# Kernel optimization log

Hardware: AMD Instinct MI355X
Metric: run time of the kernel (lower is better)

## Reference

```python
import jax, jax.numpy as jnp
import numpy as np

DIM, HEADS = 128, 8
DH = DIM // HEADS
SCALE = DH ** -0.5
N, E = 50000, 800000


def setup_inputs() -> dict:
    key = jax.random.key(0)
    ks = jax.random.split(key, 12)
    w = lambda k: jax.random.normal(k, (DIM, DIM), dtype=jnp.float32) * 0.02
    b = lambda k: jax.random.normal(k, (DIM,), dtype=jnp.float32) * 0.02
    return {
        "q_nodes": jax.random.normal(ks[0], (N, DIM), dtype=jnp.float32),
        "k_edges": jax.random.normal(ks[1], (E, DIM), dtype=jnp.float32),
        "v_edges": jax.random.normal(ks[2], (E, DIM), dtype=jnp.float32),
        "edge_index": jax.random.randint(ks[3], (2, E), 0, N, dtype=jnp.int64),
        "Wq": w(ks[4]), "bq": b(ks[5]),
        "Wk": w(ks[6]), "bk": b(ks[7]),
        "Wv": w(ks[8]), "bv": b(ks[9]),
        "Wo": w(ks[10]), "bo": b(ks[11]),
    }


def reference(q_nodes, k_edges, v_edges, edge_index, Wq, bq, Wk, bk, Wv, bv, Wo, bo):
    n, e = q_nodes.shape[0], k_edges.shape[0]
    dst = edge_index[0]  # src (edge_index[1]) is unused by the module
    q = (q_nodes @ Wq.T + bq).reshape(n, HEADS, DH)
    k = (k_edges @ Wk.T + bk).reshape(e, HEADS, DH)
    v = (v_edges @ Wv.T + bv).reshape(e, HEADS, DH)
    # per-edge score: dot(q[dst], k) per head -> [E, H]
    score = jnp.einsum('ehd,ehd->eh', q[dst], k) * SCALE
    # segment (per-dst-node) softmax over edges, numerically stable
    m = jax.ops.segment_max(score, dst, num_segments=n)          # [N, H]
    ex = jnp.exp(score - m[dst])                                  # [E, H]
    s = jax.ops.segment_sum(ex, dst, num_segments=n)             # [N, H]
    w = ex / (s[dst] + 1e-16)                                     # [E, H]
    weighted_v = (v * w[..., None]).reshape(e, DIM)               # [E, dim]
    aggr = jax.ops.segment_sum(weighted_v, dst, num_segments=n)  # [N, dim]
    return aggr @ Wo.T + bo
```

## Files before the change

### kernel.cpp

```cpp
#include <hip/hip_runtime.h>

#define TM 64
#define NTHREADS 256
#define PAD 132

typedef __attribute__((ext_vector_type(8))) short short8;
typedef __attribute__((ext_vector_type(4))) float f32x4;

__device__ __forceinline__ short f2bf(float f) {
  union { float f; unsigned u; } uf; uf.f = f;
  unsigned r = uf.u + 0x7FFFu + ((uf.u >> 16) & 1u);
  return (short)(r >> 16);
}
__device__ __forceinline__ float bf2f(short s) {
  union { unsigned u; float f; } uf; uf.u = ((unsigned)(unsigned short)s) << 16;
  return uf.f;
}
__device__ __forceinline__ short8 pack8(float4 a, float4 b) {
  short8 r;
  r[0] = f2bf(a.x); r[1] = f2bf(a.y); r[2] = f2bf(a.z); r[3] = f2bf(a.w);
  r[4] = f2bf(b.x); r[5] = f2bf(b.y); r[6] = f2bf(b.z); r[7] = f2bf(b.w);
  return r;
}


__global__ __launch_bounds__(512) void proj_mfma(
    const float* __restrict__ X, const short* __restrict__ Wb,
    const float* __restrict__ bias, float* __restrict__ Y, int M, float scale) {
  __shared__ short Xb[8192];
  int t = threadIdx.x;
  int w = t >> 6, l = t & 63, g = l >> 4, c = l & 15;
  short8 wf[4];
#pragma unroll
  for (int kc = 0; kc < 4; ++kc)
    wf[kc] = *(const short8*)(Wb + (w * 16 + c) * 128 + kc * 32 + g * 8);
  float4 b4 = *(const float4*)(bias + w * 16 + g * 4);

  for (int rb = blockIdx.x * 64; rb < M; rb += gridDim.x * 64) {
    {
      int r = t >> 3, q8 = t & 7;
      int row = rb + r; if (row >= M) row = M - 1;
      const float4* xs = (const float4*)(X + (size_t)row * 128 + q8 * 16);
      float4 x0 = xs[0], x1 = xs[1], x2 = xs[2], x3 = xs[3];
      int sw = (r & 7) << 4;
      *(short8*)((char*)Xb + r * 256 + ((q8 * 32) ^ sw)) = pack8(x0, x1);
      *(short8*)((char*)Xb + r * 256 + ((q8 * 32 + 16) ^ sw)) = pack8(x2, x3);
    }
    __syncthreads();
#pragma unroll
    for (int et = 0; et < 4; ++et) {
      int rl = et * 16 + c;
      f32x4 acc = {};
      int sw = (rl & 7) << 4;
#pragma unroll
      for (int kc = 0; kc < 4; ++kc) {
        short8 xb = *(const short8*)((char*)Xb + rl * 256 + ((kc * 64 + g * 16) ^ sw));
        acc = __builtin_amdgcn_mfma_f32_16x16x32_bf16(wf[kc], xb, acc, 0, 0, 0);
      }
      int row = rb + rl;
      if (row < M) {
        float4 o;
        o.x = (acc[0] + b4.x) * scale; o.y = (acc[1] + b4.y) * scale;
        o.z = (acc[2] + b4.z) * scale; o.w = (acc[3] + b4.w) * scale;
        *(float4*)(Y + (size_t)row * 128 + w * 16 + g * 4) = o;
      }
    }
    __syncthreads();
  }
}


__global__ __launch_bounds__(256) void hist_kernel(const int* __restrict__ dst,
                                                   int* __restrict__ cnt, int E) {
  int e = blockIdx.x * 256 + threadIdx.x;
  if (e < E) atomicAdd(&cnt[dst[e]], 1);
}

__global__ __launch_bounds__(1024) void scan_part(const int* __restrict__ cnt,
                                                  int* __restrict__ part, int N) {
  __shared__ int ws[16];
  int t = threadIdx.x, i = blockIdx.x * 1024 + t;
  int v = (i < N) ? cnt[i] : 0;
#pragma unroll
  for (int d = 1; d < 64; d <<= 1) v += __shfl_xor(v, d);
  if ((t & 63) == 0) ws[t >> 6] = v;
  __syncthreads();
  if (t < 16) {
    int x = ws[t];
#pragma unroll
    for (int d = 1; d < 16; d <<= 1) x += __shfl_xor(x, d);
    if (t == 0) part[blockIdx.x] = x;
  }
}

__global__ __launch_bounds__(64) void scan_offs(int* __restrict__ part, int P) {
  int t = threadIdx.x;
  int carry = 0;
  for (int base = 0; base < P; base += 64) {
    int i = base + t;
    int v = (i < P) ? part[i] : 0;
    int x = v;
#pragma unroll
    for (int d = 1; d < 64; d <<= 1) { int y = __shfl_up(x, d); if (t >= d) x += y; }
    if (i < P) part[i] = x - v + carry;
    carry += __shfl(x, 63);
  }
}

__global__ __launch_bounds__(1024) void scan_final(const int* __restrict__ cnt,
                                                   const int* __restrict__ part,
                                                   int* __restrict__ rp,
                                                   int* __restrict__ cur, int N) {
  __shared__ int ws[16];
  __shared__ int wofs[16];
  int t = threadIdx.x, i = blockIdx.x * 1024 + t;
  int lane = t & 63, wid = t >> 6;
  int v = (i < N) ? cnt[i] : 0;
  int x = v;
#pragma unroll
  for (int d = 1; d < 64; d <<= 1) { int y = __shfl_up(x, d); if (lane >= d) x += y; }
  if (lane == 63) ws[wid] = x;
  __syncthreads();
  if (t == 0) {
    int s = 0;
#pragma unroll
    for (int k2 = 0; k2 < 16; ++k2) { int tmp = ws[k2]; wofs[k2] = s; s += tmp; }
  }
  __syncthreads();
  int incl = x + wofs[wid] + part[blockIdx.x];
  int excl = incl - v;
  if (i < N) {
    rp[i] = excl; cur[i] = excl;
    if (i == N - 1) rp[N] = incl;
  }
}

__global__ __launch_bounds__(256) void perm_kernel(const int* __restrict__ dst,
                                                   int* __restrict__ cursor,
                                                   int* __restrict__ perm, int E) {
  int e = blockIdx.x * 256 + threadIdx.x;
  if (e < E) perm[e] = atomicAdd(&cursor[dst[e]], 1);
}

__global__ __launch_bounds__(256) void wprep4(
    const float* __restrict__ Wq, const float* __restrict__ Wk,
    const float* __restrict__ Wv, const float* __restrict__ Wo,
    short* __restrict__ wqb, short* __restrict__ wkb,
    short* __restrict__ wvb, short* __restrict__ wob) {
  int i = blockIdx.x * 256 + threadIdx.x;
  if (i < 16384) {
    wqb[i] = f2bf(Wq[i]); wkb[i] = f2bf(Wk[i]);
    wvb[i] = f2bf(Wv[i]); wob[i] = f2bf(Wo[i]);
  }
}


__global__ __launch_bounds__(512) void kproj_score(
    const float* __restrict__ K, const int* __restrict__ eidx,
    const int* __restrict__ perm, const short* __restrict__ wkb,
    const float* __restrict__ bk, const float* __restrict__ qp,
    float* __restrict__ exb, int E) {
  __shared__ short Kb[8192];
  int t = threadIdx.x;
  int w = t >> 6, l = t & 63, g = l >> 4, c = l & 15;
  short8 wK[4];
#pragma unroll
  for (int kc = 0; kc < 4; ++kc)
    wK[kc] = *(const short8*)(wkb + (w * 16 + c) * 128 + kc * 32 + g * 8);
  float4 bk4 = *(const float4*)(bk + w * 16 + g * 4);
  int r = t >> 3, q8 = t & 7;
  int b0 = r * 256 + ((q8 * 32) ^ ((r & 7) << 4));
  int stride = gridDim.x * 64;
  int eb = blockIdx.x * 64;

  float4 k0, k1, k2, k3;
  int d[4], p[4];
  {
    int row0 = eb + r; if (row0 >= E) row0 = E - 1;
    const float4* ks = (const float4*)(K + (size_t)row0 * 128 + q8 * 16);
    k0 = ks[0]; k1 = ks[1]; k2 = ks[2]; k3 = ks[3];
#pragma unroll
    for (int et = 0; et < 4; ++et) {
      int e = eb + et * 16 + c; if (e >= E) e = E - 1;
      d[et] = eidx[e]; p[et] = perm[e];
    }
  }

  for (; eb < E; eb += stride) {
    int ebn = eb + stride;
    bool hn = ebn < E;
    __syncthreads();
    *(short8*)((char*)Kb + b0) = pack8(k0, k1);
    *(short8*)((char*)Kb + (b0 ^ 16)) = pack8(k2, k3);
    float4 qv[4];
#pragma unroll
    for (int et = 0; et < 4; ++et)
      qv[et] = *(const float4*)(qp + (size_t)d[et] * 128 + w * 16 + g * 4);
    if (hn) {
      int rowk = ebn + r; if (rowk >= E) rowk = E - 1;
      const float4* ks = (const float4*)(K + (size_t)rowk * 128 + q8 * 16);
      k0 = ks[0]; k1 = ks[1]; k2 = ks[2]; k3 = ks[3];
    }
    int dn[4], pn[4];
    if (hn) {
#pragma unroll
      for (int et = 0; et < 4; ++et) {
        int e = ebn + et * 16 + c; if (e >= E) e = E - 1;
        dn[et] = eidx[e]; pn[et] = perm[e];
      }
    }
    __syncthreads();

#pragma unroll
    for (int et = 0; et < 4; ++et) {
      int eloc = et * 16 + c;
      int swr = (eloc & 7) << 4;
      f32x4 acc = {};
#pragma unroll
      for (int kc = 0; kc < 4; ++kc) {
        short8 xb = *(const short8*)((char*)Kb + eloc * 256 + ((kc * 64 + g * 16) ^ swr));
        acc = __builtin_amdgcn_mfma_f32_16x16x32_bf16(wK[kc], xb, acc, 0, 0, 0);
      }
      float s = (acc[0] + bk4.x) * qv[et].x + (acc[1] + bk4.y) * qv[et].y +
                (acc[2] + bk4.z) * qv[et].z + (acc[3] + bk4.w) * qv[et].w;
      s += __shfl_xor(s, 16);
      s += __shfl_xor(s, 32);
      if (g == 0) exb[(size_t)p[et] * 8 + w] = __expf(s);
    }
    if (hn) {
#pragma unroll
      for (int et = 0; et < 4; ++et) { d[et] = dn[et]; p[et] = pn[et]; }
    }
  }
}


__global__ __launch_bounds__(512) void vproj_weight(
    const float* __restrict__ V, const int* __restrict__ perm,
    const short* __restrict__ wvb, const float* __restrict__ exb,
    short* __restrict__ wv, int E) {
  __shared__ short Vb[8192];
  __shared__ short Ob[8192];
  int t = threadIdx.x;
  int w = t >> 6, l = t & 63, g = l >> 4, c = l & 15;
  short8 wV[4];
#pragma unroll
  for (int kc = 0; kc < 4; ++kc)
    wV[kc] = *(const short8*)(wvb + (w * 16 + c) * 128 + kc * 32 + g * 8);
  int r = t >> 3, q8 = t & 7;
  int b0 = r * 256 + ((q8 * 32) ^ ((r & 7) << 4));
  int stride = gridDim.x * 64;
  int eb = blockIdx.x * 64;

  float4 v0, v1, v2, v3;
  int p[4];
  {
    int row0 = eb + r; if (row0 >= E) row0 = E - 1;
    const float4* vs = (const float4*)(V + (size_t)row0 * 128 + q8 * 16);
    v0 = vs[0]; v1 = vs[1]; v2 = vs[2]; v3 = vs[3];
#pragma unroll
    for (int et = 0; et < 4; ++et) {
      int e = eb + et * 16 + c; if (e >= E) e = E - 1;
      p[et] = perm[e];
    }
  }

  for (; eb < E; eb += stride) {
    int ebn = eb + stride;
    bool hn = ebn < E;
    __syncthreads();
    *(short8*)((char*)Vb + b0) = pack8(v0, v1);
    *(short8*)((char*)Vb + (b0 ^ 16)) = pack8(v2, v3);
    float ev[4];
#pragma unroll
    for (int et = 0; et < 4; ++et)
      ev[et] = exb[(size_t)p[et] * 8 + w];
    int erow = eb + r; if (erow >= E) erow = E - 1;
    int prow = perm[erow];
    if (hn) {
      int rowv = ebn + r; if (rowv >= E) rowv = E - 1;
      const float4* vs = (const float4*)(V + (size_t)rowv * 128 + q8 * 16);
      v0 = vs[0]; v1 = vs[1]; v2 = vs[2]; v3 = vs[3];
    }
    int pn[4];
    if (hn) {
#pragma unroll
      for (int et = 0; et < 4; ++et) {
        int e = ebn + et * 16 + c; if (e >= E) e = E - 1;
        pn[et] = perm[e];
      }
    }
    __syncthreads();

#pragma unroll
    for (int et = 0; et < 4; ++et) {
      int eloc = et * 16 + c;
      int swr = (eloc & 7) << 4;
      f32x4 acc = {};
#pragma unroll
      for (int kc = 0; kc < 4; ++kc) {
        short8 xb = *(const short8*)((char*)Vb + eloc * 256 + ((kc * 64 + g * 16) ^ swr));
        acc = __builtin_amdgcn_mfma_f32_16x16x32_bf16(wV[kc], xb, acc, 0, 0, 0);
      }
      short4 sv;
      sv.x = f2bf(acc[0] * ev[et]); sv.y = f2bf(acc[1] * ev[et]);
      sv.z = f2bf(acc[2] * ev[et]); sv.w = f2bf(acc[3] * ev[et]);
      *(short4*)((char*)Ob + eloc * 256 + ((w * 32 + g * 8) ^ swr)) = sv;
    }
    __syncthreads();

    {
      int sw = (r & 7) << 4;
      short8 a = *(const short8*)((char*)Ob + r * 256 + ((q8 * 32) ^ sw));
      short8 b = *(const short8*)((char*)Ob + r * 256 + ((q8 * 32 + 16) ^ sw));
      *(short8*)(wv + (size_t)prow * 128 + q8 * 16) = a;
      *(short8*)(wv + (size_t)prow * 128 + q8 * 16 + 8) = b;
    }
    if (hn) {
#pragma unroll
      for (int et = 0; et < 4; ++et) p[et] = pn[et];
    }
  }
}


__global__ __launch_bounds__(256) void pull3(
    const short* __restrict__ wv, const float* __restrict__ exb,
    const int* __restrict__ rp, const float* __restrict__ bv,
    float* __restrict__ aggr, int N) {
  int w = threadIdx.x >> 6, l = threadIdx.x & 63;
  int n = blockIdx.x * 4 + w;
  if (n >= N) return;
  int beg = rp[n], end = rp[n + 1];
  int h = l >> 3;
  float a0 = 0.f, a1 = 0.f, s = 0.f;
  int j = beg;
  for (; j + 1 < end; j += 2) {
    unsigned u0 = *(const unsigned*)(wv + (size_t)j * 128 + l * 2);
    unsigned u1 = *(const unsigned*)(wv + (size_t)(j + 1) * 128 + l * 2);
    float s0 = exb[(size_t)j * 8 + h], s1 = exb[(size_t)(j + 1) * 8 + h];
    a0 += bf2f((short)(u0 & 0xFFFFu)) + bf2f((short)(u1 & 0xFFFFu));
    a1 += bf2f((short)(u0 >> 16)) + bf2f((short)(u1 >> 16));
    s += s0 + s1;
  }
  if (j < end) {
    unsigned u0 = *(const unsigned*)(wv + (size_t)j * 128 + l * 2);
    s += exb[(size_t)j * 8 + h];
    a0 += bf2f((short)(u0 & 0xFFFFu));
    a1 += bf2f((short)(u0 >> 16));
  }
  float2 o;
  if (end > beg) {
    float inv = 1.f / (s + 1e-16f);
    float2 bvv = *(const float2*)(bv + l * 2);
    o.x = a0 * inv + bvv.x; o.y = a1 * inv + bvv.y;
  } else {
    o.x = 0.f; o.y = 0.f;
  }
  *(float2*)(aggr + (size_t)n * 128 + l * 2) = o;
}


__device__ __forceinline__ void stage_x(float (*Xs)[PAD], const float* __restrict__ X,
                                        int rowbase, int M, int t) {
#pragma unroll
  for (int i = 0; i < 8; ++i) {
    int idx = t + NTHREADS * i;
    int r = idx >> 5, q = idx & 31;
    int row = rowbase + r;
    if (row >= M) row = M - 1;
    const float4 v = *(const float4*)(X + (size_t)row * 128 + q * 4);
    *(float4*)(&Xs[r][q * 4]) = v;
  }
}

__device__ __forceinline__ void gemm_tile(const float (*Xs)[PAD], float (*WT)[PAD],
                                          const float* __restrict__ W,
                                          float acc[8][4], int r0, int c0, int t) {
#pragma unroll 1
  for (int kk = 0; kk < 128; kk += 32) {
    {
      int j = t >> 1, half = t & 1;
      const float* src = W + j * 128 + kk + half * 16;
      float4 a = *(const float4*)(src);
      float4 b = *(const float4*)(src + 4);
      float4 c = *(const float4*)(src + 8);
      float4 d = *(const float4*)(src + 12);
      int cb = half * 16;
      WT[cb + 0][j] = a.x;  WT[cb + 1][j] = a.y;  WT[cb + 2][j] = a.z;  WT[cb + 3][j] = a.w;
      WT[cb + 4][j] = b.x;  WT[cb + 5][j] = b.y;  WT[cb + 6][j] = b.z;  WT[cb + 7][j] = b.w;
      WT[cb + 8][j] = c.x;  WT[cb + 9][j] = c.y;  WT[cb + 10][j] = c.z; WT[cb + 11][j] = c.w;
      WT[cb + 12][j] = d.x; WT[cb + 13][j] = d.y; WT[cb + 14][j] = d.z; WT[cb + 15][j] = d.w;
    }
    __syncthreads();
#pragma unroll
    for (int c2 = 0; c2 < 16; ++c2) {
      float4 wa = *(const float4*)(&WT[2 * c2][c0]);
      float4 wb = *(const float4*)(&WT[2 * c2 + 1][c0]);
#pragma unroll
      for (int i = 0; i < 8; ++i) {
        float2 xv = *(const float2*)(&Xs[r0 + i][kk + 2 * c2]);
        acc[i][0] = fmaf(xv.x, wa.x, acc[i][0]);
        acc[i][1] = fmaf(xv.x, wa.y, acc[i][1]);
        acc[i][2] = fmaf(xv.x, wa.z, acc[i][2]);
        acc[i][3] = fmaf(xv.x, wa.w, acc[i][3]);
        acc[i][0] = fmaf(xv.y, wb.x, acc[i][0]);
        acc[i][1] = fmaf(xv.y, wb.y, acc[i][1]);
        acc[i][2] = fmaf(xv.y, wb.z, acc[i][2]);
        acc[i][3] = fmaf(xv.y, wb.w, acc[i][3]);
      }
    }
    __syncthreads();
  }
}

__global__ __launch_bounds__(NTHREADS) void proj_kernel(
    const float* __restrict__ X, const float* __restrict__ W,
    const float* __restrict__ b, float* __restrict__ Y, int M) {
  __shared__ float Xs[TM][PAD];
  __shared__ float WT[32][PAD];
  int t = threadIdx.x;
  int B0 = blockIdx.x * TM;
  stage_x(Xs, X, B0, M, t);
  __syncthreads();
  int r0 = (t >> 5) * 8, m = t & 31, c0 = m * 4;
  float acc[8][4] = {};
  gemm_tile(Xs, WT, W, acc, r0, c0, t);
  float4 bv = ((const float4*)b)[m];
#pragma unroll
  for (int i = 0; i < 8; ++i) {
    int row = B0 + r0 + i;
    if (row < M) {
      float4 o;
      o.x = acc[i][0] + bv.x; o.y = acc[i][1] + bv.y;
      o.z = acc[i][2] + bv.z; o.w = acc[i][3] + bv.w;
      *(float4*)(Y + (size_t)row * 128 + c0) = o;
    }
  }
}

__global__ __launch_bounds__(NTHREADS) void edge_kernel(
    const float* __restrict__ Kin, const float* __restrict__ Vin,
    const int* __restrict__ eidx,
    const float* __restrict__ Wk, const float* __restrict__ bk,
    const float* __restrict__ Wv, const float* __restrict__ bv,
    const float* __restrict__ qp, float* __restrict__ s_sum,
    float* __restrict__ aggr, int E) {
  __shared__ float Xs[TM][PAD];
  __shared__ float WT[32][PAD];
  __shared__ int dsts[TM];
  int t = threadIdx.x;
  int e0 = blockIdx.x * TM;
  if (t < TM) {
    int idx = e0 + t;
    if (idx >= E) idx = E - 1;
    dsts[t] = eidx[idx];
  }
  stage_x(Xs, Kin, e0, E, t);
  __syncthreads();
  int r0 = (t >> 5) * 8, m = t & 31, c0 = m * 4;
  int h = m >> 2;
  float acc[8][4] = {};
  gemm_tile(Xs, WT, Wk, acc, r0, c0, t);
  float4 bkv = ((const float4*)bk)[m];
  float ex[8];
#pragma unroll
  for (int i = 0; i < 8; ++i) {
    int r = r0 + i;
    const float4 qv = *(const float4*)(qp + (size_t)dsts[r] * 128 + c0);
    float p = (acc[i][0] + bkv.x) * qv.x + (acc[i][1] + bkv.y) * qv.y +
              (acc[i][2] + bkv.z) * qv.z + (acc[i][3] + bkv.w) * qv.w;
    p += __shfl_xor(p, 1);
    p += __shfl_xor(p, 2);
    float e = __expf(p * 0.25f);
    ex[i] = e;
    if ((m & 3) == 0 && (e0 + r) < E)
      atomicAdd(&s_sum[(size_t)dsts[r] * 8 + h], e);
  }
  __syncthreads();
  stage_x(Xs, Vin, e0, E, t);
  __syncthreads();
#pragma unroll
  for (int i = 0; i < 8; ++i)
#pragma unroll
    for (int j = 0; j < 4; ++j) acc[i][j] = 0.f;
  gemm_tile(Xs, WT, Wv, acc, r0, c0, t);
  float4 bvv = ((const float4*)bv)[m];
#pragma unroll
  for (int i = 0; i < 8; ++i) {
    int r = r0 + i;
    if ((e0 + r) < E) {
      size_t base = (size_t)dsts[r] * 128 + c0;
      atomicAdd(&aggr[base + 0], (acc[i][0] + bvv.x) * ex[i]);
      atomicAdd(&aggr[base + 1], (acc[i][1] + bvv.y) * ex[i]);
      atomicAdd(&aggr[base + 2], (acc[i][2] + bvv.z) * ex[i]);
      atomicAdd(&aggr[base + 3], (acc[i][3] + bvv.w) * ex[i]);
    }
  }
}

__global__ __launch_bounds__(NTHREADS) void out_kernel(
    const float* __restrict__ aggr, const float* __restrict__ s_sum,
    const float* __restrict__ W, const float* __restrict__ b,
    float* __restrict__ Y, int M) {
  __shared__ float Xs[TM][PAD];
  __shared__ float WT[32][PAD];
  int t = threadIdx.x;
  int B0 = blockIdx.x * TM;
#pragma unroll
  for (int i = 0; i < 8; ++i) {
    int idx = t + NTHREADS * i;
    int r = idx >> 5, q = idx & 31;
    int row = B0 + r;
    if (row >= M) row = M - 1;
    float4 v = *(const float4*)(aggr + (size_t)row * 128 + q * 4);
    float inv = 1.0f / (s_sum[(size_t)row * 8 + (q >> 2)] + 1e-16f);
    v.x *= inv; v.y *= inv; v.z *= inv; v.w *= inv;
    *(float4*)(&Xs[r][q * 4]) = v;
  }
  __syncthreads();
  int r0 = (t >> 5) * 8, m = t & 31, c0 = m * 4;
  float acc[8][4] = {};
  gemm_tile(Xs, WT, W, acc, r0, c0, t);
  float4 bv = ((const float4*)b)[m];
#pragma unroll
  for (int i = 0; i < 8; ++i) {
    int row = B0 + r0 + i;
    if (row < M) {
      float4 o;
      o.x = acc[i][0] + bv.x; o.y = acc[i][1] + bv.y;
      o.z = acc[i][2] + bv.z; o.w = acc[i][3] + bv.w;
      *(float4*)(Y + (size_t)row * 128 + c0) = o;
    }
  }
}


extern "C" void kernel_launch(void* const* d_in, const int* in_sizes, int n_in,
                              void* d_out, int out_size, void* d_ws, size_t ws_size,
                              hipStream_t stream) {
  const float* q_nodes = (const float*)d_in[0];
  const float* k_edges = (const float*)d_in[1];
  const float* v_edges = (const float*)d_in[2];
  const int* eidx = (const int*)d_in[3];
  const float* Wq = (const float*)d_in[4];
  const float* bq = (const float*)d_in[5];
  const float* Wk = (const float*)d_in[6];
  const float* bk = (const float*)d_in[7];
  const float* Wv = (const float*)d_in[8];
  const float* bv = (const float*)d_in[9];
  const float* Wo = (const float*)d_in[10];
  const float* bo = (const float*)d_in[11];

  int N = in_sizes[0] / 128;
  int E = in_sizes[1] / 128;
  int P = (N + 1023) / 1024;

  size_t off = 0;
  auto alloc = [&](size_t b) { size_t o = off; off += (b + 255) & ~(size_t)255; return o; };
  size_t o_qp   = alloc((size_t)N * 128 * 4);
  size_t o_aggr = alloc((size_t)N * 128 * 4);
  size_t o_exb  = alloc((size_t)E * 8 * 4);
  size_t o_rp   = alloc(((size_t)N + 1) * 4);
  size_t o_cur  = alloc((size_t)N * 4);
  size_t o_cnt  = alloc((size_t)N * 4);
  size_t o_perm = alloc((size_t)E * 4);
  size_t o_part = alloc((size_t)(P + 1) * 4);
  size_t o_wqb  = alloc((size_t)16384 * 2);
  size_t o_wkb  = alloc((size_t)16384 * 2);
  size_t o_wvb  = alloc((size_t)16384 * 2);
  size_t o_wob  = alloc((size_t)16384 * 2);
  size_t o_wv   = alloc((size_t)E * 128 * 2);

  if (off <= ws_size) {
    char* base = (char*)d_ws;
    float* qp    = (float*)(base + o_qp);
    float* aggr  = (float*)(base + o_aggr);
    float* exb   = (float*)(base + o_exb);
    int*   rp    = (int*)(base + o_rp);
    int*   cur   = (int*)(base + o_cur);
    int*   cnt   = (int*)(base + o_cnt);
    int*   perm  = (int*)(base + o_perm);
    int*   part  = (int*)(base + o_part);
    short* wqb   = (short*)(base + o_wqb);
    short* wkb   = (short*)(base + o_wkb);
    short* wvb   = (short*)(base + o_wvb);
    short* wob   = (short*)(base + o_wob);
    short* wvbuf = (short*)(base + o_wv);

    hipMemsetAsync(cnt, 0, (size_t)N * 4, stream);
    wprep4<<<64, 256, 0, stream>>>(Wq, Wk, Wv, Wo, wqb, wkb, wvb, wob);
    proj_mfma<<<(N + 63) / 64, 512, 0, stream>>>(q_nodes, wqb, bq, qp, N, 0.25f);
    hist_kernel<<<(E + 255) / 256, 256, 0, stream>>>(eidx, cnt, E);
    scan_part<<<P, 1024, 0, stream>>>(cnt, part, N);
    scan_offs<<<1, 64, 0, stream>>>(part, P);
    scan_final<<<P, 1024, 0, stream>>>(cnt, part, rp, cur, N);
    perm_kernel<<<(E + 255) / 256, 256, 0, stream>>>(eidx, cur, perm, E);

    int eblk = (E + 63) / 64; if (eblk > 1024) eblk = 1024;
    kproj_score<<<eblk, 512, 0, stream>>>(k_edges, eidx, perm, wkb, bk, qp, exb, E);
    vproj_weight<<<eblk, 512, 0, stream>>>(v_edges, perm, wvb, exb, wvbuf, E);
    pull3<<<(N + 3) / 4, 256, 0, stream>>>(wvbuf, exb, rp, bv, aggr, N);
    proj_mfma<<<(N + 63) / 64, 512, 0, stream>>>(aggr, wob, bo, (float*)d_out, N, 1.0f);
  } else {
    float* q_proj = (float*)d_ws;
    float* s_sum  = q_proj + (size_t)N * 128;
    float* aggr   = s_sum + (size_t)N * 8;
    hipMemsetAsync(s_sum, 0, (size_t)N * 136 * sizeof(float), stream);
    int nblk = (N + TM - 1) / TM;
    int eblk = (E + TM - 1) / TM;
    proj_kernel<<<nblk, NTHREADS, 0, stream>>>(q_nodes, Wq, bq, q_proj, N);
    edge_kernel<<<eblk, NTHREADS, 0, stream>>>(k_edges, v_edges, eidx, Wk, bk, Wv, bv,
                                               q_proj, s_sum, aggr, E);
    out_kernel<<<nblk, NTHREADS, 0, stream>>>(aggr, s_sum, Wo, bo, (float*)d_out, N);
  }
}
```

Baseline: 448.9 us.

## Fuse V projection with segment aggregation via sorted-order atomics and fold normalization into output GEMM

The V projection kernel now walks edges in destination-sorted order, gathering V rows through an inverse permutation. Within each 64-edge tile it reduces runs of equal destination nodes in shared memory and flushes them with float atomics into raw aggregate and sum buffers. This removes the bf16 weighted-V intermediate (E×128) and the separate pull kernel. Softmax normalization and the V bias move into the output projection's load stage. The cost is scattered V row gathers and atomic contention at tile boundaries, and float atomics make the summation order nondeterministic.

New measurement: 513.7 us. 14.4% more time.

```diff
diff --git a/kernel.cpp b/kernel.cpp
--- a/kernel.cpp
+++ b/kernel.cpp
@@ -62,6 +62,66 @@
         float4 o;
         o.x = (acc[0] + b4.x) * scale; o.y = (acc[1] + b4.y) * scale;
         o.z = (acc[2] + b4.z) * scale; o.w = (acc[3] + b4.w) * scale;
+        *(float4*)(Y + (size_t)row * 128 + w * 16 + g * 4) = o;
+      }
+    }
+    __syncthreads();
+  }
+}
+
+
+__global__ __launch_bounds__(512) void proj_out_norm(
+    const float* __restrict__ araw, const float* __restrict__ sraw,
+    const float* __restrict__ bvv, const short* __restrict__ Wb,
+    const float* __restrict__ bias, float* __restrict__ Y, int M) {
+  __shared__ short Xb[8192];
+  int t = threadIdx.x;
+  int w = t >> 6, l = t & 63, g = l >> 4, c = l & 15;
+  short8 wf[4];
+#pragma unroll
+  for (int kc = 0; kc < 4; ++kc)
+    wf[kc] = *(const short8*)(Wb + (w * 16 + c) * 128 + kc * 32 + g * 8);
+  float4 b4 = *(const float4*)(bias + w * 16 + g * 4);
+
+  for (int rb = blockIdx.x * 64; rb < M; rb += gridDim.x * 64) {
+    {
+      int r = t >> 3, q8 = t & 7;
+      int row = rb + r; if (row >= M) row = M - 1;
+      float s = sraw[(size_t)row * 8 + q8];
+      const float4* as = (const float4*)(araw + (size_t)row * 128 + q8 * 16);
+      const float4* bs = (const float4*)(bvv + q8 * 16);
+      float4 x0, x1, x2, x3;
+      if (s > 0.f) {
+        float inv = 1.f / (s + 1e-16f);
+        float4 a0 = as[0], a1 = as[1], a2 = as[2], a3 = as[3];
+        float4 c0 = bs[0], c1 = bs[1], c2 = bs[2], c3 = bs[3];
+        x0.x = a0.x*inv + c0.x; x0.y = a0.y*inv + c0.y; x0.z = a0.z*inv + c0.z; x0.w = a0.w*inv + c0.w;
+        x1.x = a1.x*inv + c1.x; x1.y = a1.y*inv + c1.y; x1.z = a1.z*inv + c1.z; x1.w = a1.w*inv + c1.w;
+        x2.x = a2.x*inv + c2.x; x2.y = a2.y*inv + c2.y; x2.z = a2.z*inv + c2.z; x2.w = a2.w*inv + c2.w;
+        x3.x = a3.x*inv + c3.x; x3.y = a3.y*inv + c3.y; x3.z = a3.z*inv + c3.z; x3.w = a3.w*inv + c3.w;
+      } else {
+        x0 = {0,0,0,0}; x1 = {0,0,0,0}; x2 = {0,0,0,0}; x3 = {0,0,0,0};
+      }
+      int sw = (r & 7) << 4;
+      *(short8*)((char*)Xb + r * 256 + ((q8 * 32) ^ sw)) = pack8(x0, x1);
+      *(short8*)((char*)Xb + r * 256 + ((q8 * 32 + 16) ^ sw)) = pack8(x2, x3);
+    }
+    __syncthreads();
+#pragma unroll
+    for (int et = 0; et < 4; ++et) {
+      int rl = et * 16 + c;
+      f32x4 acc = {};
+      int sw = (rl & 7) << 4;
+#pragma unroll
+      for (int kc = 0; kc < 4; ++kc) {
+        short8 xb = *(const short8*)((char*)Xb + rl * 256 + ((kc * 64 + g * 16) ^ sw));
+        acc = __builtin_amdgcn_mfma_f32_16x16x32_bf16(wf[kc], xb, acc, 0, 0, 0);
+      }
+      int row = rb + rl;
+      if (row < M) {
+        float4 o;
+        o.x = acc[0] + b4.x; o.y = acc[1] + b4.y;
+        o.z = acc[2] + b4.z; o.w = acc[3] + b4.w;
         *(float4*)(Y + (size_t)row * 128 + w * 16 + g * 4) = o;
       }
     }
@@ -135,11 +195,17 @@
   }
 }
 
-__global__ __launch_bounds__(256) void perm_kernel(const int* __restrict__ dst,
-                                                   int* __restrict__ cursor,
-                                                   int* __restrict__ perm, int E) {
+__global__ __launch_bounds__(256) void perm_eid(const int* __restrict__ dst,
+                                                int* __restrict__ cursor,
+                                                int* __restrict__ perm,
+                                                int* __restrict__ eid,
+                                                int* __restrict__ snode, int E) {
   int e = blockIdx.x * 256 + threadIdx.x;
-  if (e < E) perm[e] = atomicAdd(&cursor[dst[e]], 1);
+  if (e < E) {
+    int d = dst[e];
+    int p = atomicAdd(&cursor[d], 1);
+    perm[e] = p; eid[p] = e; snode[p] = d;
+  }
 }
 
 __global__ __launch_bounds__(256) void wprep4(
@@ -235,60 +301,59 @@
 }
 
 
-__global__ __launch_bounds__(512) void vproj_weight(
-    const float* __restrict__ V, const int* __restrict__ perm,
-    const short* __restrict__ wvb, const float* __restrict__ exb,
-    short* __restrict__ wv, int E) {
+__global__ __launch_bounds__(512) void vpull(
+    const float* __restrict__ V, const int* __restrict__ eid,
+    const int* __restrict__ snode, const float* __restrict__ exb,
+    const short* __restrict__ wvb,
+    float* __restrict__ araw, float* __restrict__ sraw, int E) {
   __shared__ short Vb[8192];
-  __shared__ short Ob[8192];
+  __shared__ float Ob[8192];
+  __shared__ float sh_ex[512];
+  __shared__ int sh_nid[64];
   int t = threadIdx.x;
   int w = t >> 6, l = t & 63, g = l >> 4, c = l & 15;
   short8 wV[4];
 #pragma unroll
   for (int kc = 0; kc < 4; ++kc)
     wV[kc] = *(const short8*)(wvb + (w * 16 + c) * 128 + kc * 32 + g * 8);
+
   int r = t >> 3, q8 = t & 7;
   int b0 = r * 256 + ((q8 * 32) ^ ((r & 7) << 4));
-  int stride = gridDim.x * 64;
-  int eb = blockIdx.x * 64;
+  int stride = gridDim.x;
+  int tile = blockIdx.x;
+  int E8 = E * 8;
 
   float4 v0, v1, v2, v3;
-  int p[4];
+  float exc;
+  int nidc, en_;
   {
-    int row0 = eb + r; if (row0 >= E) row0 = E - 1;
-    const float4* vs = (const float4*)(V + (size_t)row0 * 128 + q8 * 16);
+    int s0 = tile * 64;
+    int ec = (s0 + r < E) ? eid[s0 + r] : 0;
+    const float4* vs = (const float4*)(V + (size_t)ec * 128 + q8 * 16);
     v0 = vs[0]; v1 = vs[1]; v2 = vs[2]; v3 = vs[3];
-#pragma unroll
-    for (int et = 0; et < 4; ++et) {
-      int e = eb + et * 16 + c; if (e >= E) e = E - 1;
-      p[et] = perm[e];
-    }
-  }
-
-  for (; eb < E; eb += stride) {
-    int ebn = eb + stride;
-    bool hn = ebn < E;
+    exc = (s0 * 8 + t < E8) ? exb[s0 * 8 + t] : 0.f;
+    nidc = (t < 64 && s0 + t < E) ? snode[s0 + t] : -1;
+    int s1 = (tile + stride) * 64;
+    en_ = (s1 + r < E) ? eid[s1 + r] : 0;
+  }
+
+  for (; tile * 64 < E; tile += stride) {
+    int tn = tile + stride;
+    int s1 = tn * 64;
+    bool hn = s1 < E;
+
     __syncthreads();
     *(short8*)((char*)Vb + b0) = pack8(v0, v1);
     *(short8*)((char*)Vb + (b0 ^ 16)) = pack8(v2, v3);
-    float ev[4];
-#pragma unroll
-    for (int et = 0; et < 4; ++et)
-      ev[et] = exb[(size_t)p[et] * 8 + w];
-    int erow = eb + r; if (erow >= E) erow = E - 1;
-    int prow = perm[erow];
+    sh_ex[t] = exc;
+    if (t < 64) sh_nid[t] = nidc;
     if (hn) {
-      int rowv = ebn + r; if (rowv >= E) rowv = E - 1;
-      const float4* vs = (const float4*)(V + (size_t)rowv * 128 + q8 * 16);
+      const float4* vs = (const float4*)(V + (size_t)en_ * 128 + q8 * 16);
       v0 = vs[0]; v1 = vs[1]; v2 = vs[2]; v3 = vs[3];
-    }
-    int pn[4];
-    if (hn) {
-#pragma unroll
-      for (int et = 0; et < 4; ++et) {
-        int e = ebn + et * 16 + c; if (e >= E) e = E - 1;
-        pn[et] = perm[e];
-      }
+      exc = (s1 * 8 + t < E8) ? exb[s1 * 8 + t] : 0.f;
+      nidc = (t < 64 && s1 + t < E) ? snode[s1 + t] : -1;
+      int s2 = (tn + stride) * 64;
+      en_ = (s2 + r < E) ? eid[s2 + r] : 0;
     }
     __syncthreads();
 
@@ -302,62 +367,39 @@
         short8 xb = *(const short8*)((char*)Vb + eloc * 256 + ((kc * 64 + g * 16) ^ swr));
         acc = __builtin_amdgcn_mfma_f32_16x16x32_bf16(wV[kc], xb, acc, 0, 0, 0);
       }
-      short4 sv;
-      sv.x = f2bf(acc[0] * ev[et]); sv.y = f2bf(acc[1] * ev[et]);
-      sv.z = f2bf(acc[2] * ev[et]); sv.w = f2bf(acc[3] * ev[et]);
-      *(short4*)((char*)Ob + eloc * 256 + ((w * 32 + g * 8) ^ swr)) = sv;
-    }
-    __syncthreads();
-
-    {
-      int sw = (r & 7) << 4;
-      short8 a = *(const short8*)((char*)Ob + r * 256 + ((q8 * 32) ^ sw));
-      short8 b = *(const short8*)((char*)Ob + r * 256 + ((q8 * 32 + 16) ^ sw));
-      *(short8*)(wv + (size_t)prow * 128 + q8 * 16) = a;
-      *(short8*)(wv + (size_t)prow * 128 + q8 * 16 + 8) = b;
-    }
-    if (hn) {
-#pragma unroll
-      for (int et = 0; et < 4; ++et) p[et] = pn[et];
-    }
-  }
-}
-
-
-__global__ __launch_bounds__(256) void pull3(
-    const short* __restrict__ wv, const float* __restrict__ exb,
-    const int* __restrict__ rp, const float* __restrict__ bv,
-    float* __restrict__ aggr, int N) {
-  int w = threadIdx.x >> 6, l = threadIdx.x & 63;
-  int n = blockIdx.x * 4 + w;
-  if (n >= N) return;
-  int beg = rp[n], end = rp[n + 1];
-  int h = l >> 3;
-  float a0 = 0.f, a1 = 0.f, s = 0.f;
-  int j = beg;
-  for (; j + 1 < end; j += 2) {
-    unsigned u0 = *(const unsigned*)(wv + (size_t)j * 128 + l * 2);
-    unsigned u1 = *(const unsigned*)(wv + (size_t)(j + 1) * 128 + l * 2);
-    float s0 = exb[(size_t)j * 8 + h], s1 = exb[(size_t)(j + 1) * 8 + h];
-    a0 += bf2f((short)(u0 & 0xFFFFu)) + bf2f((short)(u1 & 0xFFFFu));
-    a1 += bf2f((short)(u0 >> 16)) + bf2f((short)(u1 >> 16));
-    s += s0 + s1;
-  }
-  if (j < end) {
-    unsigned u0 = *(const unsigned*)(wv + (size_t)j * 128 + l * 2);
-    s += exb[(size_t)j * 8 + h];
-    a0 += bf2f((short)(u0 & 0xFFFFu));
-    a1 += bf2f((short)(u0 >> 16));
-  }
-  float2 o;
-  if (end > beg) {
-    float inv = 1.f / (s + 1e-16f);
-    float2 bvv = *(const float2*)(bv + l * 2);
-    o.x = a0 * inv + bvv.x; o.y = a1 * inv + bvv.y;
-  } else {
-    o.x = 0.f; o.y = 0.f;
-  }
-  *(float2*)(aggr + (size_t)n * 128 + l * 2) = o;
+      *(f32x4*)((char*)Ob + eloc * 512 + ((w * 64 + g * 16) ^ swr)) = acc;
+    }
+    __syncthreads();
+
+    if (t < 256) {
+      int col = t & 127, hh = t >> 7;
+      int head = col >> 4;
+      bool sflag = (col & 15) == 0;
+      float acc = 0.f, sacc = 0.f;
+      int prev = -1;
+      int jend = hh * 32 + 32;
+      for (int j = hh * 32; j < jend; ++j) {
+        int nid = sh_nid[j];
+        if (nid != prev) {
+          if (prev >= 0) {
+            atomicAdd(&araw[(size_t)prev * 128 + col], acc);
+            if (sflag) atomicAdd(&sraw[(size_t)prev * 8 + head], sacc);
+          }
+          acc = 0.f; sacc = 0.f; prev = nid;
+        }
+        if (nid >= 0) {
+          float ex = sh_ex[j * 8 + head];
+          float vv = *(const float*)((char*)Ob + j * 512 + ((col * 4) ^ ((j & 7) << 4)));
+          acc = fmaf(vv, ex, acc);
+          if (sflag) sacc += ex;
+        }
+      }
+      if (prev >= 0) {
+        atomicAdd(&araw[(size_t)prev * 128 + col], acc);
+        if (sflag) atomicAdd(&sraw[(size_t)prev * 8 + head], sacc);
+      }
+    }
+  }
 }
 
 
@@ -558,50 +600,56 @@
 
   size_t off = 0;
   auto alloc = [&](size_t b) { size_t o = off; off += (b + 255) & ~(size_t)255; return o; };
+  size_t o_cnt  = alloc((size_t)N * 4);
+  size_t o_sraw = alloc((size_t)N * 8 * 4);
+  size_t o_araw = alloc((size_t)N * 128 * 4);
+  size_t zero_end = off;
   size_t o_qp   = alloc((size_t)N * 128 * 4);
-  size_t o_aggr = alloc((size_t)N * 128 * 4);
   size_t o_exb  = alloc((size_t)E * 8 * 4);
   size_t o_rp   = alloc(((size_t)N + 1) * 4);
   size_t o_cur  = alloc((size_t)N * 4);
-  size_t o_cnt  = alloc((size_t)N * 4);
   size_t o_perm = alloc((size_t)E * 4);
+  size_t o_eid  = alloc((size_t)E * 4);
+  size_t o_snd  = alloc((size_t)E * 4);
   size_t o_part = alloc((size_t)(P + 1) * 4);
   size_t o_wqb  = alloc((size_t)16384 * 2);
   size_t o_wkb  = alloc((size_t)16384 * 2);
   size_t o_wvb  = alloc((size_t)16384 * 2);
   size_t o_wob  = alloc((size_t)16384 * 2);
-  size_t o_wv   = alloc((size_t)E * 128 * 2);
 
   if (off <= ws_size) {
     char* base = (char*)d_ws;
+    int*   cnt   = (int*)(base + o_cnt);
+    float* sraw  = (float*)(base + o_sraw);
+    float* araw  = (float*)(base + o_araw);
     float* qp    = (float*)(base + o_qp);
-    float* aggr  = (float*)(base + o_aggr);
     float* exb   = (float*)(base + o_exb);
     int*   rp    = (int*)(base + o_rp);
     int*   cur   = (int*)(base + o_cur);
-    int*   cnt   = (int*)(base + o_cnt);
     int*   perm  = (int*)(base + o_perm);
+    int*   eid   = (int*)(base + o_eid);
+    int*   snd   = (int*)(base + o_snd);
     int*   part  = (int*)(base + o_part);
     short* wqb   = (short*)(base + o_wqb);
     short* wkb   = (short*)(base + o_wkb);
     short* wvb   = (short*)(base + o_wvb);
     short* wob   = (short*)(base + o_wob);
-    short* wvbuf = (short*)(base + o_wv);
-
-    hipMemsetAsync(cnt, 0, (size_t)N * 4, stream);
+
+    hipMemsetAsync(base + o_cnt, 0, zero_end - o_cnt, stream);
     wprep4<<<64, 256, 0, stream>>>(Wq, Wk, Wv, Wo, wqb, wkb, wvb, wob);
     proj_mfma<<<(N + 63) / 64, 512, 0, stream>>>(q_nodes, wqb, bq, qp, N, 0.25f);
     hist_kernel<<<(E + 255) / 256, 256, 0, stream>>>(eidx, cnt, E);
     scan_part<<<P, 1024, 0, stream>>>(cnt, part, N);
     scan_offs<<<1, 64, 0, stream>>>(part, P);
     scan_final<<<P, 1024, 0, stream>>>(cnt, part, rp, cur, N);
-    perm_kernel<<<(E + 255) / 256, 256, 0, stream>>>(eidx, cur, perm, E);
-
-    int eblk = (E + 63) / 64; if (eblk > 1024) eblk = 1024;
-    kproj_score<<<eblk, 512, 0, stream>>>(k_edges, eidx, perm, wkb, bk, qp, exb, E);
-    vproj_weight<<<eblk, 512, 0, stream>>>(v_edges, perm, wvb, exb, wvbuf, E);
-    pull3<<<(N + 3) / 4, 256, 0, stream>>>(wvbuf, exb, rp, bv, aggr, N);
-    proj_mfma<<<(N + 63) / 64, 512, 0, stream>>>(aggr, wob, bo, (float*)d_out, N, 1.0f);
+    perm_eid<<<(E + 255) / 256, 256, 0, stream>>>(eidx, cur, perm, eid, snd, E);
+
+    int kblk = (E + 63) / 64; if (kblk > 1024) kblk = 1024;
+    kproj_score<<<kblk, 512, 0, stream>>>(k_edges, eidx, perm, wkb, bk, qp, exb, E);
+    int vblk = (E + 63) / 64; if (vblk > 768) vblk = 768;
+    vpull<<<vblk, 512, 0, stream>>>(v_edges, eid, snd, exb, wvb, araw, sraw, E);
+    proj_out_norm<<<(N + 63) / 64, 512, 0, stream>>>(araw, sraw, bv, wob, bo,
+                                                     (float*)d_out, N);
   } else {
     float* q_proj = (float*)d_ws;
     float* s_sum  = q_proj + (size_t)N * 128;
```
